# Kernel optimization log

Measured on AMD Instinct MI355X. Metric: run time of the kernel, lower is better.

The kernel has to match this reference:

```python
import jax, jax.numpy as jnp
import numpy as np

EMBED = 1024
HEADS = 16
HEAD_DIM = EMBED // HEADS
SCALE = HEAD_DIM ** -0.5


def setup_inputs() -> dict:
    key = jax.random.key(0)
    ks = jax.random.split(key, 11)
    B, S, D = 2, 2048, EMBED
    s = D ** -0.5
    return {
        "Q": jax.random.normal(ks[0], (B, S, D), jnp.float32),
        "K": jax.random.normal(ks[1], (B, S, D), jnp.float32),
        "V": jax.random.normal(ks[2], (B, S, D), jnp.float32),
        "Wq": jax.random.normal(ks[3], (D, D), jnp.float32) * s,
        "bq": jax.random.normal(ks[4], (D,), jnp.float32) * 0.01,
        "Wk": jax.random.normal(ks[5], (D, D), jnp.float32) * s,
        "bk": jax.random.normal(ks[6], (D,), jnp.float32) * 0.01,
        "Wv": jax.random.normal(ks[7], (D, D), jnp.float32) * s,
        "bv": jax.random.normal(ks[8], (D,), jnp.float32) * 0.01,
        "Wo": jax.random.normal(ks[9], (D, D), jnp.float32) * s,
        "bo": jax.random.normal(ks[10], (D,), jnp.float32) * 0.01,
    }


def reference(Q, K, V, Wq, bq, Wk, bk, Wv, bv, Wo, bo):
    N, S, D = Q.shape
    H, Hd = HEADS, HEAD_DIM
    # linear projections (x @ W + b), then split heads: [N, S, H, Hd]
    q = (Q @ Wq + bq).reshape(N, S, H, Hd)
    k = (K @ Wk + bk).reshape(N, S, H, Hd)
    v = (V @ Wv + bv).reshape(N, S, H, Hd)
    # scaled dot-product attention, full [N,H,S,S] scores as in the original
    energy = jnp.einsum('nqhd,nkhd->nhqk', q, k) * SCALE
    attn = jax.nn.softmax(energy, axis=3)
    out = jnp.einsum('nhql,nlhd->nqhd', attn, v).reshape(N, S, D)
    return out @ Wo + bo
```

## Files before the change

kernel.cpp:

```cpp
#include <hip/hip_runtime.h>
#include <cstdint>


typedef _Float16 h4 __attribute__((ext_vector_type(4)));
typedef _Float16 h8 __attribute__((ext_vector_type(8)));
typedef float f4 __attribute__((ext_vector_type(4)));
typedef float f16v __attribute__((ext_vector_type(16)));
typedef unsigned int u32x4 __attribute__((ext_vector_type(4)));
typedef const unsigned int __attribute__((address_space(1)))* gp1_t;
typedef unsigned int __attribute__((address_space(3)))* lp3_t;

#define FSWZ(r) ((((r) ^ ((r) >> 3))) & 7)

__device__ __forceinline__ void gld_lds16(const void* g, const void* l) {
  __builtin_amdgcn_global_load_lds((gp1_t)(uintptr_t)g,
                                   (lp3_t)(unsigned int)(uintptr_t)l, 16, 0, 0);
}
__device__ __forceinline__ unsigned pkh(float a, float b) {
  return __builtin_bit_cast(unsigned, __builtin_amdgcn_cvt_pkrtz(a, b));
}
__device__ __forceinline__ void plswap(unsigned& a, unsigned& b) {
  asm volatile("v_permlane32_swap_b32 %0, %1" : "+v"(a), "+v"(b));
}


__global__ void cvt_x3(const float* __restrict__ a, const float* __restrict__ b,
                       const float* __restrict__ c, _Float16* __restrict__ out) {
  const int z = blockIdx.z;
  const float* in = (z == 0) ? a : (z == 1) ? b : c;
  _Float16* o = out + (size_t)z * 4194304;
  const int i = (blockIdx.x * 256 + threadIdx.x) * 8;
  float4 u = *(const float4*)(in + i);
  float4 w = *(const float4*)(in + i + 4);
  h8 r = {(_Float16)u.x, (_Float16)u.y, (_Float16)u.z, (_Float16)u.w,
          (_Float16)w.x, (_Float16)w.y, (_Float16)w.z, (_Float16)w.w};
  *(h8*)(o + i) = r;
}

__global__ void cvt_w4(const float* __restrict__ wq, const float* __restrict__ wk,
                       const float* __restrict__ wv, const float* __restrict__ wo,
                       _Float16* __restrict__ WT) {
  const int z = blockIdx.z;
  const float* W = (z == 0) ? wq : (z == 1) ? wk : (z == 2) ? wv : wo;
  _Float16* o = WT + (size_t)z * 1048576;
  const int k = blockIdx.x * 256 + threadIdx.x;
  const int n0 = blockIdx.y * 4;
  float4 w = *(const float4*)(W + (size_t)k * 1024 + n0);
  o[(size_t)(n0 + 0) * 1024 + k] = (_Float16)w.x;
  o[(size_t)(n0 + 1) * 1024 + k] = (_Float16)w.y;
  o[(size_t)(n0 + 2) * 1024 + k] = (_Float16)w.z;
  o[(size_t)(n0 + 3) * 1024 + k] = (_Float16)w.w;
}


#define G_STAGE(BUF, KT)                                                       \
  do {                                                                         \
    _Pragma("unroll") for (int rr_ = 0; rr_ < 4; ++rr_) {                      \
      const int idx_ = rr_ * 256 + tid;                                        \
      const int r_ = idx_ >> 3, g_ = idx_ & 7;                                 \
      const int lb_ = (rr_ * 256 + wave * 64) * 8;                             \
      gld_lds16(A16 + (size_t)(row0 + r_) * 1024 + (KT) * 64 + (g_ ^ FSWZ(r_)) * 8,\
                &As[BUF][lb_]);                                                \
      gld_lds16(Bt + (size_t)(col0 + r_) * 1024 + (KT) * 64 + (g_ ^ FSWZ(r_)) * 8,\
                &Bs[BUF][lb_]);                                                \
    }                                                                          \
  } while (0)

__global__ __launch_bounds__(256, 2) void gemm_qkv(const _Float16* __restrict__ X16,
                                                   const _Float16* __restrict__ WT,
                                                   const float* __restrict__ bq,
                                                   const float* __restrict__ bk,
                                                   const float* __restrict__ bv,
                                                   _Float16* __restrict__ qkv16) {
  __shared__ _Float16 As[2][8192];
  __shared__ _Float16 Bs[2][8192];
  const int z = blockIdx.z;
  const _Float16* A16 = X16 + (size_t)z * 4194304;
  const _Float16* Bt = WT + (size_t)z * 1048576;
  const float* bias = (z == 0) ? bq : (z == 1) ? bk : bv;
  _Float16* out16 = qkv16 + (size_t)z * 4194304;
  const float scl = (z == 0) ? 0.18033688f : 1.0f;
  const int tid = threadIdx.x;
  const int wave = tid >> 6, lane = tid & 63;
  const int lg = lane >> 4, ll = lane & 15;
  const int wr = wave >> 1, wc = wave & 1;
  const int row0 = blockIdx.x * 128, col0 = blockIdx.y * 128;
  f4 acc[4][4] = {};
  G_STAGE(0, 0);
  __syncthreads();
  int cur = 0;
  for (int kt = 0; kt < 16; ++kt) {
    if (kt + 1 < 16) G_STAGE(cur ^ 1, kt + 1);
#pragma unroll
    for (int kk = 0; kk < 2; ++kk) {
      h8 af[4], bf[4];
#pragma unroll
      for (int mi = 0; mi < 4; ++mi) {
        const int r = wr * 64 + mi * 16 + ll;
        af[mi] = *(const h8*)&As[cur][r * 64 + (((kk * 4 + lg) ^ FSWZ(r)) << 3)];
      }
#pragma unroll
      for (int ni = 0; ni < 4; ++ni) {
        const int r = wc * 64 + ni * 16 + ll;
        bf[ni] = *(const h8*)&Bs[cur][r * 64 + (((kk * 4 + lg) ^ FSWZ(r)) << 3)];
      }
#pragma unroll
      for (int mi = 0; mi < 4; ++mi)
#pragma unroll
        for (int ni = 0; ni < 4; ++ni)
          acc[mi][ni] = __builtin_amdgcn_mfma_f32_16x16x32_f16(af[mi], bf[ni],
                                                               acc[mi][ni], 0, 0, 0);
    }
    __syncthreads();
    cur ^= 1;
  }
  if (z == 2) {
#pragma unroll
    for (int ni = 0; ni < 4; ++ni) {
      const int c = col0 + wc * 64 + ni * 16 + ll;
      const float bv = bias[c];
      const int h = c >> 6, hd = c & 63;
#pragma unroll
      for (int mi = 0; mi < 4; ++mi) {
        const int r = row0 + wr * 64 + mi * 16 + lg * 4;
        const int b = r >> 11, s = r & 2047;
        h4 w = {(_Float16)(acc[mi][ni][0] + bv), (_Float16)(acc[mi][ni][1] + bv),
                (_Float16)(acc[mi][ni][2] + bv), (_Float16)(acc[mi][ni][3] + bv)};
        *(h4*)(out16 + ((size_t)((b * 16 + h) * 64 + hd)) * 2048 + s) = w;
      }
    }
  } else {
#pragma unroll
    for (int ni = 0; ni < 4; ++ni) {
      const int c = col0 + wc * 64 + ni * 16 + ll;
      const float bv = bias[c];
#pragma unroll
      for (int mi = 0; mi < 4; ++mi) {
#pragma unroll
        for (int i = 0; i < 4; ++i) {
          const int r = row0 + wr * 64 + mi * 16 + lg * 4 + i;
          const float val = (acc[mi][ni][i] + bv) * scl;
          const int b = r >> 11, s = r & 2047, h = c >> 6, hd = c & 63;
          out16[((size_t)((b * 16 + h) * 2048 + s)) * 64 + hd] = (_Float16)val;
        }
      }
    }
  }
}


#define GO_STAGE(BUF, KT)                                                      \
  do {                                                                         \
    _Pragma("unroll") for (int rr_ = 0; rr_ < 4; ++rr_) {                      \
      const int idx_ = rr_ * 256 + tid;                                        \
      const int r_ = idx_ >> 3, g_ = idx_ & 7;                                 \
      gld_lds16(A16 + (size_t)(row0 + r_) * 1024 + (KT) * 64 + (g_ ^ FSWZ(r_)) * 8,\
                &As[BUF][(rr_ * 256 + wave * 64) * 8]);                        \
    }                                                                          \
    _Pragma("unroll") for (int rr_ = 0; rr_ < 2; ++rr_) {                      \
      const int idx_ = rr_ * 256 + tid;                                        \
      const int r_ = idx_ >> 3, g_ = idx_ & 7;                                 \
      gld_lds16(WoT + (size_t)(col0 + r_) * 1024 + (KT) * 64 + (g_ ^ FSWZ(r_)) * 8,\
                &Bs[BUF][(rr_ * 256 + wave * 64) * 8]);                        \
    }                                                                          \
  } while (0)

__global__ __launch_bounds__(256, 3) void gemm_out_k(const _Float16* __restrict__ A16,
                                                     const _Float16* __restrict__ WoT,
                                                     const float* __restrict__ bo,
                                                     float* __restrict__ out) {
  __shared__ _Float16 As[2][8192];
  __shared__ _Float16 Bs[2][4096];
  const int tid = threadIdx.x;
  const int wave = tid >> 6, lane = tid & 63;
  const int lg = lane >> 4, ll = lane & 15;
  const int wr = wave >> 1, wc = wave & 1;
  const int row0 = blockIdx.x * 128, col0 = blockIdx.y * 64;
  f4 acc[4][2] = {};
  GO_STAGE(0, 0);
  __syncthreads();
  int cur = 0;
  for (int kt = 0; kt < 16; ++kt) {
    if (kt + 1 < 16) GO_STAGE(cur ^ 1, kt + 1);
#pragma unroll
    for (int kk = 0; kk < 2; ++kk) {
      h8 af[4], bf[2];
#pragma unroll
      for (int mi = 0; mi < 4; ++mi) {
        const int r = wr * 64 + mi * 16 + ll;
        af[mi] = *(const h8*)&As[cur][r * 64 + (((kk * 4 + lg) ^ FSWZ(r)) << 3)];
      }
#pragma unroll
      for (int ni = 0; ni < 2; ++ni) {
        const int r = wc * 32 + ni * 16 + ll;
        bf[ni] = *(const h8*)&Bs[cur][r * 64 + (((kk * 4 + lg) ^ FSWZ(r)) << 3)];
      }
#pragma unroll
      for (int mi = 0; mi < 4; ++mi)
#pragma unroll
        for (int ni = 0; ni < 2; ++ni)
          acc[mi][ni] = __builtin_amdgcn_mfma_f32_16x16x32_f16(af[mi], bf[ni],
                                                               acc[mi][ni], 0, 0, 0);
    }
    __syncthreads();
    cur ^= 1;
  }
#pragma unroll
  for (int ni = 0; ni < 2; ++ni) {
    const int c = col0 + wc * 32 + ni * 16 + ll;
    const float bv = bo[c];
#pragma unroll
    for (int mi = 0; mi < 4; ++mi)
#pragma unroll
      for (int i = 0; i < 4; ++i) {
        const int r = row0 + wr * 64 + mi * 16 + lg * 4 + i;
        out[(size_t)r * 1024 + c] = acc[mi][ni][i] + bv;
      }
  }
}


#define STAGE_K(BUF, KT)                                                      \
  do {                                                                        \
    _Pragma("unroll") for (int rr_ = 0; rr_ < 2; ++rr_) {                     \
      const int idx_ = rr_ * 256 + tid;                                       \
      const int r_ = idx_ >> 3, g_ = idx_ & 7;                                \
      gld_lds16(kbp + (size_t)((KT) * 64 + r_) * 64 + ((g_ ^ FSWZ(r_)) * 8),  \
                &Ks[BUF][(rr_ * 256 + wave * 64) * 8]);                       \
    }                                                                         \
  } while (0)

#define STAGE_V(BUF, KT)                                                      \
  do {                                                                        \
    _Pragma("unroll") for (int rr_ = 0; rr_ < 2; ++rr_) {                     \
      const int idx_ = rr_ * 256 + tid;                                       \
      const int r_ = idx_ >> 3, g_ = idx_ & 7;                                \
      gld_lds16(vtp + (size_t)r_ * 2048 + (KT) * 64 + ((g_ ^ FSWZ(r_)) * 8),  \
                &Vt[BUF][(rr_ * 256 + wave * 64) * 8]);                       \
    }                                                                         \
  } while (0)

#define QK_COMPUTE(BUF, S0, S1)                                               \
  do {                                                                        \
    S0 = (f16v){};                                                            \
    S1 = (f16v){};                                                            \
    _Pragma("unroll") for (int kc_ = 0; kc_ < 4; ++kc_) {                     \
      const int c_ = kc_ * 2 + hi;                                            \
      h8 k0_ = *(const h8*)&Ks[BUF][l31 * 64 + ((c_ ^ FSWZ(l31)) << 3)];      \
      h8 k1_ = *(const h8*)&Ks[BUF][(32 + l31) * 64 +                         \
                                    ((c_ ^ FSWZ(32 + l31)) << 3)];            \
      h8 qf_ = (kc_ == 0) ? qf0 : (kc_ == 1) ? qf1 : (kc_ == 2) ? qf2 : qf3;  \
      S0 = __builtin_amdgcn_mfma_f32_32x32x16_f16(k0_, qf_, S0, 0, 0, 0);     \
      S1 = __builtin_amdgcn_mfma_f32_32x32x16_f16(k1_, qf_, S1, 0, 0, 0);     \
    }                                                                         \
  } while (0)

#define PACK_AF(DST, SX, PP)                                                  \
  do {                                                                        \
    unsigned wA = pkh(SX[(PP) + 0], SX[(PP) + 1]);                            \
    unsigned wB = pkh(SX[(PP) + 2], SX[(PP) + 3]);                            \
    unsigned wC = pkh(SX[(PP) + 4], SX[(PP) + 5]);                            \
    unsigned wD = pkh(SX[(PP) + 6], SX[(PP) + 7]);                            \
    plswap(wA, wC);                                                           \
    plswap(wB, wD);                                                           \
    DST = (u32x4){wA, wB, wC, wD};                                            \
  } while (0)

#define SM_PK(S0, S1)                                                         \
  do {                                                                        \
    float t_[8];                                                              \
    _Pragma("unroll") for (int j2_ = 0; j2_ < 8; ++j2_)                       \
        t_[j2_] = fmaxf(fmaxf(S0[j2_], S0[j2_ + 8]),                          \
                        fmaxf(S1[j2_], S1[j2_ + 8]));                         \
    float pm_ = fmaxf(fmaxf(fmaxf(t_[0], t_[1]), fmaxf(t_[2], t_[3])),        \
                      fmaxf(fmaxf(t_[4], t_[5]), fmaxf(t_[6], t_[7])));       \
    pm_ = fmaxf(pm_, __shfl_xor(pm_, 32));                                    \
    if (__any(pm_ > mval + 8.0f)) {                                           \
      const float mn_ = fmaxf(mval, pm_);                                     \
      const float f_ = __builtin_amdgcn_exp2f(mval - mn_);                    \
      mval = mn_;                                                             \
      Fb[wave][l31] = f_;                                                     \
      const f4 fr0_ = *(const f4*)&Fb[wave][0 + 4 * hi];                      \
      const f4 fr1_ = *(const f4*)&Fb[wave][8 + 4 * hi];                      \
      const f4 fr2_ = *(const f4*)&Fb[wave][16 + 4 * hi];                     \
      const f4 fr3_ = *(const f4*)&Fb[wave][24 + 4 * hi];                     \
      _Pragma("unroll") for (int r_ = 0; r_ < 16; ++r_) {                     \
        const float fx_ =                                                     \
            (r_ < 4 ? fr0_ : r_ < 8 ? fr1_ : r_ < 12 ? fr2_ : fr3_)[r_ & 3];  \
        acc0[r_] *= fx_;                                                      \
        acc1[r_] *= fx_;                                                      \
        accS[r_] *= fx_;                                                      \
      }                                                                       \
    }                                                                         \
    _Pragma("unroll") for (int r_ = 0; r_ < 16; ++r_) {                       \
      S0[r_] = __builtin_amdgcn_exp2f(S0[r_] - mval);                         \
      S1[r_] = __builtin_amdgcn_exp2f(S1[r_] - mval);                         \
    }                                                                         \
    PACK_AF(afr[0], S0, 0);                                                   \
    PACK_AF(afr[1], S0, 8);                                                   \
    PACK_AF(afr[2], S1, 0);                                                   \
    PACK_AF(afr[3], S1, 8);                                                   \
  } while (0)

#define PV_APPLY(BUF)                                                         \
  do {                                                                        \
    _Pragma("unroll") for (int i_ = 0; i_ < 4; ++i_) {                        \
      const int c_ = i_ * 2 + hi;                                             \
      h8 vf0_ = *(const h8*)&Vt[BUF][l31 * 64 + ((c_ ^ FSWZ(l31)) << 3)];     \
      h8 vf1_ = *(const h8*)&Vt[BUF][(32 + l31) * 64 +                        \
                                     ((c_ ^ FSWZ(32 + l31)) << 3)];           \
      h8 af_ = __builtin_bit_cast(h8, afr[i_]);                               \
      acc0 = __builtin_amdgcn_mfma_f32_32x32x16_f16(af_, vf0_, acc0, 0, 0, 0);\
      acc1 = __builtin_amdgcn_mfma_f32_32x32x16_f16(af_, vf1_, acc1, 0, 0, 0);\
      accS = __builtin_amdgcn_mfma_f32_32x32x16_f16(af_, vone, accS, 0, 0, 0);\
    }                                                                         \
  } while (0)

__global__ __launch_bounds__(256, 2) void attn_kernel(
    const _Float16* __restrict__ q16, const _Float16* __restrict__ k16,
    const _Float16* __restrict__ v16t, _Float16* __restrict__ aout) {
  __shared__ _Float16 Ks[3][4096];
  __shared__ _Float16 Vt[3][4096];
  __shared__ float Fb[4][32];
  const int tid = threadIdx.x;
  const int wave = tid >> 6, lane = tid & 63;
  const int l31 = lane & 31, hi = lane >> 5;
  const int blk = blockIdx.x;
  const int xcd = blk & 7, j = blk >> 3;
  const int bh = xcd * 4 + (j >> 4);
  const int qb = j & 15;
  const int q0w = qb * 128 + wave * 32;
  const _Float16* qbp = q16 + (size_t)bh * 131072;
  const _Float16* kbp = k16 + (size_t)bh * 131072;
  const _Float16* vtp = v16t + (size_t)bh * 131072;

  h8 qf0 = *(const h8*)(qbp + (size_t)(q0w + l31) * 64 + 0 + hi * 8);
  h8 qf1 = *(const h8*)(qbp + (size_t)(q0w + l31) * 64 + 16 + hi * 8);
  h8 qf2 = *(const h8*)(qbp + (size_t)(q0w + l31) * 64 + 32 + hi * 8);
  h8 qf3 = *(const h8*)(qbp + (size_t)(q0w + l31) * 64 + 48 + hi * 8);

  const h8 vone = {(_Float16)1.f, (_Float16)1.f, (_Float16)1.f, (_Float16)1.f,
                   (_Float16)1.f, (_Float16)1.f, (_Float16)1.f, (_Float16)1.f};
  f16v acc0 = {}, acc1 = {}, accS = {};
  f16v sr0, sr1;
  u32x4 afr[4];
  float mval = -1e30f;

  STAGE_K(0, 0);
  STAGE_V(0, 0);
  STAGE_K(1, 1);
  STAGE_V(1, 1);
  __syncthreads();
  QK_COMPUTE(0, sr0, sr1);
  SM_PK(sr0, sr1);

  int s0 = 0, s1 = 1, s2 = 2;
  for (int t = 0; t < 31; ++t) {
    if (t < 30) { STAGE_K(s2, t + 2); STAGE_V(s2, t + 2); }
    __builtin_amdgcn_s_setprio(1);
    QK_COMPUTE(s1, sr0, sr1);
    PV_APPLY(s0);
    __builtin_amdgcn_s_setprio(0);
    SM_PK(sr0, sr1);
    __syncthreads();
    const int tmp = s0; s0 = s1; s1 = s2; s2 = tmp;
  }
  PV_APPLY(s0);

  const int b = bh >> 4, h = bh & 15;
#pragma unroll
  for (int r = 0; r < 16; ++r) {
    const float fx = 1.0f / accS[r];
    const int srow = q0w + (r & 3) + 8 * (r >> 2) + 4 * hi;
    _Float16* op = aout + ((size_t)(b * 2048 + srow)) * 1024 + h * 64 + l31;
    op[0] = (_Float16)(acc0[r] * fx);
    op[32] = (_Float16)(acc1[r] * fx);
  }
}


extern "C" void kernel_launch(void* const* d_in, const int* in_sizes, int n_in,
                              void* d_out, int out_size, void* d_ws, size_t ws_size,
                              hipStream_t stream) {
  const float* Q  = (const float*)d_in[0];
  const float* K  = (const float*)d_in[1];
  const float* V  = (const float*)d_in[2];
  const float* Wq = (const float*)d_in[3];
  const float* bq = (const float*)d_in[4];
  const float* Wk = (const float*)d_in[5];
  const float* bk = (const float*)d_in[6];
  const float* Wv = (const float*)d_in[7];
  const float* bv = (const float*)d_in[8];
  const float* Wo = (const float*)d_in[9];
  const float* bo = (const float*)d_in[10];

  _Float16* H      = (_Float16*)d_ws;
  _Float16* X16    = H;
  _Float16* WT     = H + 12582912;
  _Float16* qkv16  = H + 16777216;
  _Float16* aout16 = H + 29360128;
  float* out = (float*)d_out;

  cvt_x3<<<dim3(2048, 1, 3), 256, 0, stream>>>(Q, K, V, X16);
  cvt_w4<<<dim3(4, 256, 4), 256, 0, stream>>>(Wq, Wk, Wv, Wo, WT);
  gemm_qkv<<<dim3(32, 8, 3), 256, 0, stream>>>(X16, WT, bq, bk, bv, qkv16);
  attn_kernel<<<dim3(512), 256, 0, stream>>>(qkv16, qkv16 + 4194304,
                                             qkv16 + 8388608, aout16);
  gemm_out_k<<<dim3(32, 16), 256, 0, stream>>>(aout16, WT + 3145728, bo, out);
}
```

Before: 126.7 us.

## Enlarge output GEMM tile to 128x128 and unroll attention ring-buffer loop by three

The output projection GEMM now uses 128x128 tiles instead of 128x64, so each block loads a larger B tile and each wave holds a 4x4 accumulator grid. This raises data reuse per LDS load and halves the grid, at the cost of more registers and LDS and lower occupancy (launch bounds drop from 3 to 2). The attention main loop is unrolled by three so the triple-buffer indices become compile-time constants, which removes the rotation arithmetic and the conditional staging. The last two iterations are peeled out.

Result: no change. 126.0 us (-0.6%).

```diff
diff --git a/kernel.cpp b/kernel.cpp
--- a/kernel.cpp
+++ b/kernel.cpp
@@ -154,29 +154,26 @@
     _Pragma("unroll") for (int rr_ = 0; rr_ < 4; ++rr_) {                      \
       const int idx_ = rr_ * 256 + tid;                                        \
       const int r_ = idx_ >> 3, g_ = idx_ & 7;                                 \
+      const int lb_ = (rr_ * 256 + wave * 64) * 8;                             \
       gld_lds16(A16 + (size_t)(row0 + r_) * 1024 + (KT) * 64 + (g_ ^ FSWZ(r_)) * 8,\
-                &As[BUF][(rr_ * 256 + wave * 64) * 8]);                        \
+                &As[BUF][lb_]);                                                \
+      gld_lds16(WoT + (size_t)(col0 + r_) * 1024 + (KT) * 64 + (g_ ^ FSWZ(r_)) * 8,\
+                &Bs[BUF][lb_]);                                                \
     }                                                                          \
-    _Pragma("unroll") for (int rr_ = 0; rr_ < 2; ++rr_) {                      \
-      const int idx_ = rr_ * 256 + tid;                                        \
-      const int r_ = idx_ >> 3, g_ = idx_ & 7;                                 \
-      gld_lds16(WoT + (size_t)(col0 + r_) * 1024 + (KT) * 64 + (g_ ^ FSWZ(r_)) * 8,\
-                &Bs[BUF][(rr_ * 256 + wave * 64) * 8]);                        \
-    }                                                                          \
-  } while (0)
-
-__global__ __launch_bounds__(256, 3) void gemm_out_k(const _Float16* __restrict__ A16,
+  } while (0)
+
+__global__ __launch_bounds__(256, 2) void gemm_out_k(const _Float16* __restrict__ A16,
                                                      const _Float16* __restrict__ WoT,
                                                      const float* __restrict__ bo,
                                                      float* __restrict__ out) {
   __shared__ _Float16 As[2][8192];
-  __shared__ _Float16 Bs[2][4096];
+  __shared__ _Float16 Bs[2][8192];
   const int tid = threadIdx.x;
   const int wave = tid >> 6, lane = tid & 63;
   const int lg = lane >> 4, ll = lane & 15;
   const int wr = wave >> 1, wc = wave & 1;
-  const int row0 = blockIdx.x * 128, col0 = blockIdx.y * 64;
-  f4 acc[4][2] = {};
+  const int row0 = blockIdx.x * 128, col0 = blockIdx.y * 128;
+  f4 acc[4][4] = {};
   GO_STAGE(0, 0);
   __syncthreads();
   int cur = 0;
@@ -184,21 +181,21 @@
     if (kt + 1 < 16) GO_STAGE(cur ^ 1, kt + 1);
 #pragma unroll
     for (int kk = 0; kk < 2; ++kk) {
-      h8 af[4], bf[2];
+      h8 af[4], bf[4];
 #pragma unroll
       for (int mi = 0; mi < 4; ++mi) {
         const int r = wr * 64 + mi * 16 + ll;
         af[mi] = *(const h8*)&As[cur][r * 64 + (((kk * 4 + lg) ^ FSWZ(r)) << 3)];
       }
 #pragma unroll
-      for (int ni = 0; ni < 2; ++ni) {
-        const int r = wc * 32 + ni * 16 + ll;
+      for (int ni = 0; ni < 4; ++ni) {
+        const int r = wc * 64 + ni * 16 + ll;
         bf[ni] = *(const h8*)&Bs[cur][r * 64 + (((kk * 4 + lg) ^ FSWZ(r)) << 3)];
       }
 #pragma unroll
       for (int mi = 0; mi < 4; ++mi)
 #pragma unroll
-        for (int ni = 0; ni < 2; ++ni)
+        for (int ni = 0; ni < 4; ++ni)
           acc[mi][ni] = __builtin_amdgcn_mfma_f32_16x16x32_f16(af[mi], bf[ni],
                                                                acc[mi][ni], 0, 0, 0);
     }
@@ -206,8 +203,8 @@
     cur ^= 1;
   }
 #pragma unroll
-  for (int ni = 0; ni < 2; ++ni) {
-    const int c = col0 + wc * 32 + ni * 16 + ll;
+  for (int ni = 0; ni < 4; ++ni) {
+    const int c = col0 + wc * 64 + ni * 16 + ll;
     const float bv = bo[c];
 #pragma unroll
     for (int mi = 0; mi < 4; ++mi)
@@ -316,6 +313,18 @@
     }                                                                         \
   } while (0)
 
+#define ATTN_ITER(T, A, B, C)                                                 \
+  do {                                                                        \
+    STAGE_K(C, (T) + 2);                                                      \
+    STAGE_V(C, (T) + 2);                                                      \
+    __builtin_amdgcn_s_setprio(1);                                            \
+    QK_COMPUTE(B, sr0, sr1);                                                  \
+    PV_APPLY(A);                                                              \
+    __builtin_amdgcn_s_setprio(0);                                            \
+    SM_PK(sr0, sr1);                                                          \
+    __syncthreads();                                                          \
+  } while (0)
+
 __global__ __launch_bounds__(256, 2) void attn_kernel(
     const _Float16* __restrict__ q16, const _Float16* __restrict__ k16,
     const _Float16* __restrict__ v16t, _Float16* __restrict__ aout) {
@@ -354,18 +363,17 @@
   QK_COMPUTE(0, sr0, sr1);
   SM_PK(sr0, sr1);
 
-  int s0 = 0, s1 = 1, s2 = 2;
-  for (int t = 0; t < 31; ++t) {
-    if (t < 30) { STAGE_K(s2, t + 2); STAGE_V(s2, t + 2); }
-    __builtin_amdgcn_s_setprio(1);
-    QK_COMPUTE(s1, sr0, sr1);
-    PV_APPLY(s0);
-    __builtin_amdgcn_s_setprio(0);
-    SM_PK(sr0, sr1);
-    __syncthreads();
-    const int tmp = s0; s0 = s1; s1 = s2; s2 = tmp;
-  }
-  PV_APPLY(s0);
+  for (int tb = 0; tb < 30; tb += 3) {
+    ATTN_ITER(tb + 0, 0, 1, 2);
+    ATTN_ITER(tb + 1, 1, 2, 0);
+    ATTN_ITER(tb + 2, 2, 0, 1);
+  }
+  __builtin_amdgcn_s_setprio(1);
+  QK_COMPUTE(1, sr0, sr1);
+  PV_APPLY(0);
+  __builtin_amdgcn_s_setprio(0);
+  SM_PK(sr0, sr1);
+  PV_APPLY(1);
 
   const int b = bh >> 4, h = bh & 15;
 #pragma unroll
@@ -406,5 +414,5 @@
   gemm_qkv<<<dim3(32, 8, 3), 256, 0, stream>>>(X16, WT, bq, bk, bv, qkv16);
   attn_kernel<<<dim3(512), 256, 0, stream>>>(qkv16, qkv16 + 4194304,
                                              qkv16 + 8388608, aout16);
-  gemm_out_k<<<dim3(32, 16), 256, 0, stream>>>(aout16, WT + 3145728, bo, out);
-}
+  gemm_out_k<<<dim3(32, 8), 256, 0, stream>>>(aout16, WT + 3145728, bo, out);
+}
```
